# Kernel optimization log

Hardware: AMD Instinct MI355X
Metric: run time of the kernel (lower is better)

Reference implementation:

```python
import jax, jax.numpy as jnp
import numpy as np

DIM = 768
HEADS = 8

def setup_inputs() -> dict:
    key = jax.random.key(0)
    k1, k2, k3, k4 = jax.random.split(key, 4)
    x = jax.random.normal(k1, (4, 2048, DIM), dtype=jnp.float32)
    # torch Linear(D, 3D, bias=False): weight [3D, D]; store transposed [D, 3D]
    W_qkv = jax.random.normal(k2, (DIM, 3 * DIM), dtype=jnp.float32) * (DIM ** -0.5)
    W_o = jax.random.normal(k3, (DIM, DIM), dtype=jnp.float32) * (DIM ** -0.5)
    b_o = jax.random.normal(k4, (DIM,), dtype=jnp.float32) * 0.01
    return {"x": x, "W_qkv": W_qkv, "W_o": W_o, "b_o": b_o}

def reference(x, W_qkv, W_o, b_o):
    B, N, D = x.shape
    H = HEADS
    dh = D // H
    scale = dh ** -0.5
    qkv = x @ W_qkv                                   # [B, N, 3D]
    qkv = qkv.reshape(B, N, 3, H, dh)
    qkv = jnp.transpose(qkv, (2, 0, 3, 1, 4))         # [3, B, H, N, dh]
    Q, K, V = qkv[0], qkv[1], qkv[2]
    scores = jnp.einsum('bhqd,bhkd->bhqk', Q, K) * scale  # [B, H, N, N]
    attn = jax.nn.softmax(scores, axis=-1)
    out = jnp.einsum('bhqk,bhkd->bhqd', attn, V)      # [B, H, N, dh]
    # Faithful to original: reshape [B,H,N,dh] -> [B,N,D] WITHOUT head transpose
    out = out.reshape(B, N, D)
    return out @ W_o + b_o
```

## Files before the change

### kernel.cpp

```cpp
#include <hip/hip_runtime.h>

typedef __attribute__((ext_vector_type(8))) short short8;
typedef __attribute__((ext_vector_type(4))) float f32x4;
typedef __attribute__((ext_vector_type(4))) _Float16 half4;
typedef __attribute__((ext_vector_type(2))) __fp16 fp16x2;

#define B_SZ 4
#define NSEQ 2048
#define DIM  768
#define NH   8
#define DH   96

__device__ __forceinline__ unsigned short f2bf(float f) {
  unsigned int u = __float_as_uint(f);
  u += 0x7fffu + ((u >> 16) & 1u);
  return (unsigned short)(u >> 16);
}

__device__ __forceinline__ float fexp2(float x) {
#if __has_builtin(__builtin_amdgcn_exp2f)
  return __builtin_amdgcn_exp2f(x);
#else
  return exp2f(x);
#endif
}

__device__ __forceinline__ void glds16(const void* g, void* l) {
  __builtin_amdgcn_global_load_lds((const __attribute__((address_space(1))) void*)g,
                                   (__attribute__((address_space(3))) void*)l, 16, 0, 0);
}

__global__ __launch_bounds__(256) void cvt_x_kernel(const float* __restrict__ x,
                                                    unsigned short* __restrict__ xb) {
  int i = blockIdx.x * 256 + threadIdx.x;
  float4 v = ((const float4*)x)[i];
  ushort4 o;
  o.x = f2bf(v.x); o.y = f2bf(v.y); o.z = f2bf(v.z); o.w = f2bf(v.w);
  ((ushort4*)xb)[i] = o;
}

__global__ __launch_bounds__(256) void transpose_cvt_kernel(const float* __restrict__ W,
                                                            unsigned short* __restrict__ WT,
                                                            int ncols) {
  __shared__ float tile[32][33];
  int tx = threadIdx.x, ty = threadIdx.y;
  int c0 = blockIdx.x * 32;
  int r0 = blockIdx.y * 32;
#pragma unroll
  for (int i = 0; i < 4; i++)
    tile[ty + i * 8][tx] = W[(size_t)(r0 + ty + i * 8) * ncols + c0 + tx];
  __syncthreads();
#pragma unroll
  for (int i = 0; i < 4; i++)
    WT[(size_t)(c0 + ty + i * 8) * 768 + r0 + tx] = f2bf(tile[tx][ty + i * 8]);
}

template <int EPI>
__global__ __launch_bounds__(256) void gemm_bt(
    const unsigned short* __restrict__ A, const unsigned short* __restrict__ Bt,
    unsigned short* __restrict__ qo, unsigned short* __restrict__ ko,
    _Float16* __restrict__ vo, float* __restrict__ fo,
    const float* __restrict__ bias)
{
  __shared__ unsigned short As[128 * 32];
  __shared__ unsigned short Bs[128 * 32];
  const int t = threadIdx.x;
  const int w = t >> 6, lane = t & 63;
  const int l15 = lane & 15, qd = lane >> 4;
  const int m0 = blockIdx.y * 128, n0 = blockIdx.x * 128;
  const int wm = (w >> 1) * 64, wn = (w & 1) * 64;

  const int sr = lane >> 2;
  const int sc = (lane & 3) * 8;
  const unsigned short* ga = A  + (size_t)(m0 + w * 16 + sr) * DIM + sc;
  const unsigned short* gb = Bt + (size_t)(n0 + w * 16 + sr) * DIM + sc;

  f32x4 acc[4][4] = {};

  for (int k0 = 0; k0 < DIM; k0 += 32) {
    glds16(ga + k0,            &As[w * 512]);
    glds16(ga + 64 * DIM + k0, &As[(4 + w) * 512]);
    glds16(gb + k0,            &Bs[w * 512]);
    glds16(gb + 64 * DIM + k0, &Bs[(4 + w) * 512]);
    __syncthreads();
    short8 af[4], bfr[4];
#pragma unroll
    for (int i = 0; i < 4; i++)
      af[i]  = *(const short8*)&As[(wm + i * 16 + l15) * 32 + qd * 8];
#pragma unroll
    for (int i = 0; i < 4; i++)
      bfr[i] = *(const short8*)&Bs[(wn + i * 16 + l15) * 32 + qd * 8];
#pragma unroll
    for (int mi = 0; mi < 4; mi++)
#pragma unroll
      for (int ni = 0; ni < 4; ni++)
        acc[mi][ni] = __builtin_amdgcn_mfma_f32_16x16x32_bf16(af[mi], bfr[ni], acc[mi][ni], 0, 0, 0);
    __syncthreads();
  }

#pragma unroll
  for (int mi = 0; mi < 4; mi++)
#pragma unroll
    for (int ni = 0; ni < 4; ni++) {
      int rowb = m0 + wm + mi * 16 + qd * 4;
      int col  = n0 + wn + ni * 16 + l15;
      if (EPI == 0) {
        int b = rowb >> 11, n = rowb & 2047;
        int s = col / DIM;
        int rem = col - s * DIM;
        int hh = rem / DH;
        int c = rem - hh * DH;
        size_t bh = (size_t)(b * NH + hh);
        if (s == 2) {
          half4 pk;
#pragma unroll
          for (int r = 0; r < 4; r++) pk[r] = (_Float16)acc[mi][ni][r];
          *(half4*)&vo[(bh * DH + c) * NSEQ + n] = pk;
        } else if (s == 0) {
#pragma unroll
          for (int r = 0; r < 4; r++)
            qo[(bh * NSEQ + n + r) * DH + c] = f2bf(acc[mi][ni][r] * 0.1472444679f);
        } else {
#pragma unroll
          for (int r = 0; r < 4; r++)
            ko[(bh * NSEQ + n + r) * DH + c] = f2bf(acc[mi][ni][r]);
        }
      } else {
#pragma unroll
        for (int r = 0; r < 4; r++)
          fo[(size_t)(rowb + r) * DIM + col] = acc[mi][ni][r] + bias[col];
      }
    }
}

__global__ __launch_bounds__(256, 4) void flash_kernel(
    const unsigned short* __restrict__ Qb, const unsigned short* __restrict__ Kb,
    const _Float16* __restrict__ Vtb, unsigned short* __restrict__ Z)
{
  constexpr int VSTR = 72;
  __shared__ unsigned short Ks[64 * 96];
  __shared__ _Float16 Vs[96 * VSTR];

  const int t = threadIdx.x, w = t >> 6, lane = t & 63;
  const int l15 = lane & 15, qd = lane >> 4;
  const int swz = (l15 >> 1) & 3;
  const int qt = blockIdx.x, h = blockIdx.y, b = blockIdx.z;
  const size_t bh = (size_t)(b * NH + h);
  const unsigned short* Qg = Qb + (bh * NSEQ + (size_t)qt * 64) * DH;
  const unsigned short* Kg = Kb + bh * NSEQ * DH;
  const _Float16*       Vg = Vtb + bh * (size_t)DH * NSEQ;

  int srcoff[3];
#pragma unroll
  for (int i = 0; i < 3; i++) {
    int L = w * 192 + i * 64 + lane;
    int r = L / 12, c = L - r * 12;
    srcoff[i] = r * 96 + ((c ^ ((r >> 1) & 3)) * 8);
  }

#pragma unroll
  for (int i = 0; i < 3; i++)
    glds16(Qg + srcoff[i], &Ks[w * 1536 + i * 512]);
  __syncthreads();
  short8 qa[3];
#pragma unroll
  for (int ks = 0; ks < 3; ks++)
    qa[ks] = *(const short8*)&Ks[(w * 16 + l15) * 96 + ((ks * 4 + qd) ^ swz) * 8];

  f32x4 o[7] = {};
  float mprev = -1e30f;
  const half4 onef = {(_Float16)1.f, (_Float16)1.f, (_Float16)1.f, (_Float16)1.f};

  for (int kt = 0; kt < 32; kt++) {
    __syncthreads();
    const unsigned short* Kt = Kg + (size_t)kt * 64 * DH;
#pragma unroll
    for (int i = 0; i < 3; i++)
      glds16(Kt + srcoff[i], &Ks[w * 1536 + i * 512]);
    const _Float16* Vt = Vg + kt * 64;
#pragma unroll
    for (int i = 0; i < 3; i++) {
      int idx = t + i * 256;
      int r = idx >> 3, oo = idx & 7;
      *(float4*)&Vs[r * VSTR + oo * 8] = *(const float4*)(Vt + (size_t)r * NSEQ + oo * 8);
    }
    __syncthreads();

    f32x4 s[4] = {};
#pragma unroll
    for (int ks = 0; ks < 3; ks++)
#pragma unroll
      for (int fk = 0; fk < 4; fk++) {
        short8 kf = *(const short8*)&Ks[(fk * 16 + l15) * 96 + ((ks * 4 + qd) ^ swz) * 8];
        s[fk] = __builtin_amdgcn_mfma_f32_16x16x32_bf16(kf, qa[ks], s[fk], 0, 0, 0);
      }

    float mx = fmaxf(fmaxf(s[0][0], s[0][1]), fmaxf(s[0][2], s[0][3]));
#pragma unroll
    for (int fk = 1; fk < 4; fk++)
      mx = fmaxf(mx, fmaxf(fmaxf(s[fk][0], s[fk][1]), fmaxf(s[fk][2], s[fk][3])));
    mx = fmaxf(mx, __shfl_xor(mx, 16, 64));
    mx = fmaxf(mx, __shfl_xor(mx, 32, 64));
    float mnew = fmaxf(mprev, mx);
    float alpha = fexp2(mprev - mnew);
    mprev = mnew;

    half4 pf[4];
#pragma unroll
    for (int fk = 0; fk < 4; fk++) {
      union { fp16x2 h2[2]; half4 h4; } u;
      u.h2[0] = __builtin_amdgcn_cvt_pkrtz(fexp2(s[fk][0] - mnew), fexp2(s[fk][1] - mnew));
      u.h2[1] = __builtin_amdgcn_cvt_pkrtz(fexp2(s[fk][2] - mnew), fexp2(s[fk][3] - mnew));
      pf[fk] = u.h4;
    }
#pragma unroll
    for (int i = 0; i < 7; i++) o[i] = o[i] * alpha;

#pragma unroll
    for (int fk = 0; fk < 4; fk++) {
#pragma unroll
      for (int fc = 0; fc < 6; fc++) {
        half4 vf = *(const half4*)&Vs[(fc * 16 + l15) * VSTR + fk * 16 + qd * 4];
        o[fc] = __builtin_amdgcn_mfma_f32_16x16x16f16(vf, pf[fk], o[fc], 0, 0, 0);
      }
      o[6] = __builtin_amdgcn_mfma_f32_16x16x16f16(onef, pf[fk], o[6], 0, 0, 0);
    }
  }

  float inv = 1.0f / o[6][0];
  int q = qt * 64 + w * 16 + l15;
  size_t zbase = ((size_t)b * NSEQ + h * 256 + (q >> 3)) * DIM + (q & 7) * DH;
#pragma unroll
  for (int fc = 0; fc < 6; fc++)
#pragma unroll
    for (int r = 0; r < 4; r += 2) {
      unsigned int pkd = (unsigned int)f2bf(o[fc][r] * inv)
                       | ((unsigned int)f2bf(o[fc][r + 1] * inv) << 16);
      *(unsigned int*)&Z[zbase + fc * 16 + qd * 4 + r] = pkd;
    }
}

extern "C" void kernel_launch(void* const* d_in, const int* in_sizes, int n_in,
                              void* d_out, int out_size, void* d_ws, size_t ws_size,
                              hipStream_t stream)
{
  (void)in_sizes; (void)n_in; (void)out_size; (void)ws_size;
  const float* x    = (const float*)d_in[0];
  const float* Wqkv = (const float*)d_in[1];
  const float* Wo   = (const float*)d_in[2];
  const float* bo   = (const float*)d_in[3];
  float* out = (float*)d_out;

  unsigned short* ws    = (unsigned short*)d_ws;
  unsigned short* xb    = ws;
  unsigned short* wqkvT = xb    + (size_t)8192 * 768;
  unsigned short* woT   = wqkvT + (size_t)2304 * 768;
  unsigned short* Qw    = woT   + (size_t)768 * 768;
  unsigned short* Kw    = Qw    + (size_t)6291456;
  _Float16*       Vw    = (_Float16*)(Kw + (size_t)6291456);
  unsigned short* Zw    = (unsigned short*)(Vw + (size_t)6291456);

  cvt_x_kernel<<<6144, 256, 0, stream>>>(x, xb);
  transpose_cvt_kernel<<<dim3(72, 24), dim3(32, 8), 0, stream>>>(Wqkv, wqkvT, 2304);
  transpose_cvt_kernel<<<dim3(24, 24), dim3(32, 8), 0, stream>>>(Wo, woT, 768);
  gemm_bt<0><<<dim3(18, 64), 256, 0, stream>>>(xb, wqkvT, Qw, Kw, Vw, nullptr, nullptr);
  flash_kernel<<<dim3(32, 8, 4), 256, 0, stream>>>(Qw, Kw, Vw, Zw);
  gemm_bt<1><<<dim3(6, 64), 256, 0, stream>>>(Zw, woT, nullptr, nullptr, nullptr, out, bo);
}
```

Before: 255.4 us.

## Use 16x16x32 f16 MFMA for PV with permuted key rows and async V loads

```diff
diff --git a/kernel.cpp b/kernel.cpp
--- a/kernel.cpp
+++ b/kernel.cpp
@@ -3,6 +3,7 @@
 typedef __attribute__((ext_vector_type(8))) short short8;
 typedef __attribute__((ext_vector_type(4))) float f32x4;
 typedef __attribute__((ext_vector_type(4))) _Float16 half4;
+typedef __attribute__((ext_vector_type(8))) _Float16 half8;
 typedef __attribute__((ext_vector_type(2))) __fp16 fp16x2;
 
 #define B_SZ 4
@@ -137,30 +138,39 @@
     const unsigned short* __restrict__ Qb, const unsigned short* __restrict__ Kb,
     const _Float16* __restrict__ Vtb, unsigned short* __restrict__ Z)
 {
-  constexpr int VSTR = 72;
   __shared__ unsigned short Ks[64 * 96];
-  __shared__ _Float16 Vs[96 * VSTR];
+  __shared__ _Float16 Vs[96 * 64];
 
   const int t = threadIdx.x, w = t >> 6, lane = t & 63;
   const int l15 = lane & 15, qd = lane >> 4;
   const int swz = (l15 >> 1) & 3;
+  const int vswz = l15 & 7;
   const int qt = blockIdx.x, h = blockIdx.y, b = blockIdx.z;
   const size_t bh = (size_t)(b * NH + h);
   const unsigned short* Qg = Qb + (bh * NSEQ + (size_t)qt * 64) * DH;
   const unsigned short* Kg = Kb + bh * NSEQ * DH;
   const _Float16*       Vg = Vtb + bh * (size_t)DH * NSEQ;
 
-  int srcoff[3];
+  int koff[3];
 #pragma unroll
   for (int i = 0; i < 3; i++) {
     int L = w * 192 + i * 64 + lane;
     int r = L / 12, c = L - r * 12;
-    srcoff[i] = r * 96 + ((c ^ ((r >> 1) & 3)) * 8);
+    int fk = r >> 4, m = r & 15;
+    int key = 32 * (fk & 1) + 4 * (fk >> 1) + 8 * (m >> 2) + (m & 3);
+    koff[i] = key * 96 + ((c ^ ((r >> 1) & 3)) * 8);
+  }
+  int voff[3];
+#pragma unroll
+  for (int i = 0; i < 3; i++) {
+    int L = i * 256 + t;
+    int r = L >> 3, c = L & 7;
+    voff[i] = r * NSEQ + ((c ^ (r & 7)) * 8);
   }
 
 #pragma unroll
   for (int i = 0; i < 3; i++)
-    glds16(Qg + srcoff[i], &Ks[w * 1536 + i * 512]);
+    glds16(Qg + koff[i], &Ks[w * 1536 + i * 512]);
   __syncthreads();
   short8 qa[3];
 #pragma unroll
@@ -169,21 +179,19 @@
 
   f32x4 o[7] = {};
   float mprev = -1e30f;
-  const half4 onef = {(_Float16)1.f, (_Float16)1.f, (_Float16)1.f, (_Float16)1.f};
+  const half8 onef = {(_Float16)1.f, (_Float16)1.f, (_Float16)1.f, (_Float16)1.f,
+                      (_Float16)1.f, (_Float16)1.f, (_Float16)1.f, (_Float16)1.f};
 
   for (int kt = 0; kt < 32; kt++) {
     __syncthreads();
     const unsigned short* Kt = Kg + (size_t)kt * 64 * DH;
 #pragma unroll
     for (int i = 0; i < 3; i++)
-      glds16(Kt + srcoff[i], &Ks[w * 1536 + i * 512]);
+      glds16(Kt + koff[i], &Ks[w * 1536 + i * 512]);
     const _Float16* Vt = Vg + kt * 64;
 #pragma unroll
-    for (int i = 0; i < 3; i++) {
-      int idx = t + i * 256;
-      int r = idx >> 3, oo = idx & 7;
-      *(float4*)&Vs[r * VSTR + oo * 8] = *(const float4*)(Vt + (size_t)r * NSEQ + oo * 8);
-    }
+    for (int i = 0; i < 3; i++)
+      glds16(Vt + voff[i], &Vs[(i * 256 + w * 64) * 8]);
     __syncthreads();
 
     f32x4 s[4] = {};
@@ -217,18 +225,21 @@
     for (int i = 0; i < 7; i++) o[i] = o[i] * alpha;
 
 #pragma unroll
-    for (int fk = 0; fk < 4; fk++) {
+    for (int p = 0; p < 2; p++) {
+      union { half4 h4[2]; half8 h8; } bu;
+      bu.h4[0] = pf[p]; bu.h4[1] = pf[p + 2];
 #pragma unroll
       for (int fc = 0; fc < 6; fc++) {
-        half4 vf = *(const half4*)&Vs[(fc * 16 + l15) * VSTR + fk * 16 + qd * 4];
-        o[fc] = __builtin_amdgcn_mfma_f32_16x16x16f16(vf, pf[fk], o[fc], 0, 0, 0);
+        half8 vf = *(const half8*)&Vs[(fc * 16 + l15) * 64 + ((p * 4 + qd) ^ vswz) * 8];
+        o[fc] = __builtin_amdgcn_mfma_f32_16x16x32_f16(vf, bu.h8, o[fc], 0, 0, 0);
       }
-      o[6] = __builtin_amdgcn_mfma_f32_16x16x16f16(onef, pf[fk], o[6], 0, 0, 0);
+      o[6] = __builtin_amdgcn_mfma_f32_16x16x32_f16(onef, bu.h8, o[6], 0, 0, 0);
     }
   }
 
   float inv = 1.0f / o[6][0];
-  int q = qt * 64 + w * 16 + l15;
+  int qloc = 32 * (w & 1) + 4 * (w >> 1) + 8 * (l15 >> 2) + (l15 & 3);
+  int q = qt * 64 + qloc;
   size_t zbase = ((size_t)b * NSEQ + h * 256 + (q >> 3)) * DIM + (q & 7) * DH;
 #pragma unroll
   for (int fc = 0; fc < 6; fc++)
```

After: 240.7 us. -5.7%, faster.
